# Performance work log

Measured on AMD Instinct MI355X. Metric: run time of the kernel, lower is better.

Reference implementation:

```python
import jax, jax.numpy as jnp
import numpy as np

H = 1024      # hidden_dim
P = 8         # n_paths
K = 2         # top_k
THR = 0.1     # firing_threshold
B = 16384     # batch of tokens


def setup_inputs() -> dict:
    key = jax.random.key(0)
    ks = jax.random.split(key, 8)
    g = lambda k, shape, s=0.02: (jax.random.normal(k, shape, dtype=jnp.float32) * s)
    return {
        "x": jax.random.normal(ks[0], (B, H), dtype=jnp.float32),
        # PathGate: Linear(H, H//2) -> SiLU -> Linear(H//2, P), softmax
        "gate_w1": g(ks[1], (H, H // 2)),
        "gate_b1": jnp.zeros((H // 2,), jnp.float32),
        "gate_w2": g(ks[2], (H // 2, P)),
        "gate_b2": jnp.zeros((P,), jnp.float32),
        # each path: Linear(H,H)+SiLU (stacked over P)
        "path_w": g(ks[3], (P, H, H)),
        "path_b": jnp.zeros((P, H), jnp.float32),
        # out_projs: Linear(H,H,bias=False) per path
        "proj_w": g(ks[4], (P, H, H)),
        # blend scalar parameter (init 0.0 -> alpha = 0.5)
        "blend": jnp.zeros((), jnp.float32),
    }


def reference(x, gate_w1, gate_b1, gate_w2, gate_b2, path_w, path_b, proj_w, blend):
    Bn = x.shape[0]
    # gate probabilities (B, P)
    h = jax.nn.silu(x @ gate_w1 + gate_b1)
    gate = jax.nn.softmax(h @ gate_w2 + gate_b2, axis=-1)

    # hard top-k with firing threshold -> per-token per-path combine weight
    vals, idx = jax.lax.top_k(gate, K)              # (B, K)
    fired = vals > THR                              # (B, K)
    w = jnp.zeros_like(gate).at[jnp.arange(Bn)[:, None], idx].add(
        jnp.where(fired, vals, 0.0))                # (B, P) sparse combine weights

    # path compute (dense over P; same values as masked per-path dispatch)
    path_out = jax.nn.silu(jnp.einsum('bh,phd->pbd', x, path_w) + path_b[:, None, :])
    proj_out = jnp.einsum('pbd,pdo->pbo', path_out, proj_w)   # (P, B, H)

    combined = jnp.einsum('bp,pbo->bo', w, proj_out)          # weighted scatter-combine
    total = w.sum(axis=-1)                                    # (B,)
    has_fired = total > 0
    denom = jnp.where(has_fired, total, 1.0)[:, None]
    combined = jnp.where(has_fired[:, None], combined / denom, x)

    alpha = jax.nn.sigmoid(blend)
    out = alpha * combined + (1.0 - alpha) * x
    return out, gate
```

## Files before the change

kernel.cpp:

```cpp
#include <hip/hip_runtime.h>
#include <hip/hip_bf16.h>
#include <cstdint>

#define B_TOK 16384
#define HDIM  1024
#define HGATE 512
#define NPATH 8
#define THRV  0.1f
#define RESSCALE 512.0f
#define MAXROWS (2 * B_TOK + NPATH * 128)

typedef __bf16 bf16x8 __attribute__((ext_vector_type(8)));
typedef _Float16 f16x8 __attribute__((ext_vector_type(8)));
typedef float  f32x4  __attribute__((ext_vector_type(4)));
typedef unsigned short u16;

__device__ __forceinline__ u16 f2bf(float f) {
    uint32_t u = __float_as_uint(f);
    u += 0x7fff + ((u >> 16) & 1);
    return (u16)(u >> 16);
}
__device__ __forceinline__ float bf2f(u16 v) {
    return __uint_as_float((uint32_t)v << 16);
}
union H16 { _Float16 h; u16 u; };
__device__ __forceinline__ u16 f2h(float f) { H16 t; t.h = (_Float16)f; return t.u; }
__device__ __forceinline__ float h2f(u16 b) { H16 t; t.u = b; return (float)t.h; }
__device__ __forceinline__ float silu_f(float a) {
    return a / (1.0f + expf(-a));
}
__device__ __forceinline__ f32x4 mfma_bf16(bf16x8 a, bf16x8 b, f32x4 c) {
    return __builtin_amdgcn_mfma_f32_16x16x32_bf16(a, b, c, 0, 0, 0);
}
__device__ __forceinline__ f32x4 mfma_f16(f16x8 a, f16x8 b, f32x4 c) {
    return __builtin_amdgcn_mfma_f32_16x16x32_f16(a, b, c, 0, 0, 0);
}
__device__ __forceinline__ void async_lds16(const u16* g, u16* l) {
    __builtin_amdgcn_global_load_lds((const __attribute__((address_space(1))) uint32_t*)g,
                                     (__attribute__((address_space(3))) uint32_t*)l,
                                     16, 0, 0);
}

#define PIPE_WAIT_BARRIER(N)                                             \
    do {                                                                 \
        asm volatile("s_waitcnt vmcnt(" #N ")\n\ts_barrier" ::: "memory"); \
        __builtin_amdgcn_sched_barrier(0);                               \
    } while (0)
#define PIPE_BARRIER() asm volatile("s_barrier" ::: "memory")

#define SWZ(r) (((r) >> 1) & 3)

__global__ void k_convert_x(const float* __restrict__ x, u16* __restrict__ xb,
                            u16* __restrict__ xh, u16* __restrict__ xl) {
    int i = (blockIdx.x * 256 + threadIdx.x) * 4;
    float4 v = *(const float4*)(x + i);
    float vv[4] = {v.x, v.y, v.z, v.w};
    u16 hb[4], hh[4], hl[4];
    #pragma unroll
    for (int c = 0; c < 4; c++) {
        hb[c] = f2bf(vv[c]);
        u16 hi = f2h(vv[c]);
        hh[c] = hi;
        hl[c] = f2h((vv[c] - h2f(hi)) * RESSCALE);
    }
    uint2 ob, oh, ol;
    ob.x = (uint32_t)hb[0] | ((uint32_t)hb[1] << 16);
    ob.y = (uint32_t)hb[2] | ((uint32_t)hb[3] << 16);
    oh.x = (uint32_t)hh[0] | ((uint32_t)hh[1] << 16);
    oh.y = (uint32_t)hh[2] | ((uint32_t)hh[3] << 16);
    ol.x = (uint32_t)hl[0] | ((uint32_t)hl[1] << 16);
    ol.y = (uint32_t)hl[2] | ((uint32_t)hl[3] << 16);
    *(uint2*)(xb + i) = ob;
    *(uint2*)(xh + i) = oh;
    *(uint2*)(xl + i) = ol;
}

__global__ void k_transpose_bf16(const float* __restrict__ W, u16* __restrict__ WT) {
    __shared__ float tile[32][33];
    int p = blockIdx.z;
    const float* Wp = W + (size_t)p * HDIM * HDIM;
    u16* WTp = WT + (size_t)p * HDIM * HDIM;
    int d0 = blockIdx.x * 32, h0 = blockIdx.y * 32;
    int tx = threadIdx.x, ty = threadIdx.y;
    #pragma unroll
    for (int rr = 0; rr < 4; rr++) {
        int r = ty + rr * 8;
        tile[r][tx] = Wp[(size_t)(h0 + r) * HDIM + d0 + tx];
    }
    __syncthreads();
    #pragma unroll
    for (int rr = 0; rr < 4; rr++) {
        int r = ty + rr * 8;
        WTp[(size_t)(d0 + r) * HDIM + h0 + tx] = f2bf(tile[tx][r]);
    }
}

__global__ void k_split_w1(const float* __restrict__ W1, u16* __restrict__ WhT,
                           u16* __restrict__ WlT) {
    __shared__ float tile[32][33];
    int n0 = blockIdx.x * 32, k0 = blockIdx.y * 32;
    int tx = threadIdx.x, ty = threadIdx.y;
    #pragma unroll
    for (int rr = 0; rr < 4; rr++) {
        int r = ty + rr * 8;
        tile[r][tx] = W1[(size_t)(k0 + r) * HGATE + n0 + tx];
    }
    __syncthreads();
    #pragma unroll
    for (int rr = 0; rr < 4; rr++) {
        int r = ty + rr * 8;
        float v = tile[tx][r];
        u16 hi = f2h(v);
        WhT[(size_t)(n0 + r) * HDIM + k0 + tx] = hi;
        WlT[(size_t)(n0 + r) * HDIM + k0 + tx] = f2h((v - h2f(hi)) * RESSCALE);
    }
}

__global__ __launch_bounds__(256) void k_gate_mfma(const u16* __restrict__ Ah,
                                                   const u16* __restrict__ Al,
                                                   const u16* __restrict__ BhT,
                                                   const u16* __restrict__ BlT,
                                                   const float* __restrict__ b1,
                                                   float* __restrict__ Hout) {
    __shared__ __align__(16) u16 smem[32768];
    int t = threadIdx.x;
    int m0 = blockIdx.x * 128, n0 = blockIdx.y * 128;
    int wave = t >> 6, lane = t & 63;
    int quad = lane >> 4, l16 = lane & 15;
    int wr = (wave >> 1) * 64, wc = (wave & 1) * 64;
    f32x4 acc[4][4] = {};
    f32x4 accm[4][4] = {};
    union UV { uint4 u; f16x8 v; };
    int rb = t >> 2;
    int cs = ((t & 3) ^ SWZ(rb)) * 8;
    int wb = wave * 512;

    int offA[4], offB[4];
    #pragma unroll
    for (int i = 0; i < 4; i++) {
        int rA = wr + i * 16 + l16;
        offA[i] = rA * 32 + (quad ^ SWZ(rA)) * 8;
        int rB = wc + i * 16 + l16;
        offB[i] = rB * 32 + (quad ^ SWZ(rB)) * 8;
    }

    const u16* pAh0 = Ah + (size_t)(m0 + rb) * HDIM + cs;
    const u16* pAh1 = Ah + (size_t)(m0 + 64 + rb) * HDIM + cs;
    const u16* pAl0 = Al + (size_t)(m0 + rb) * HDIM + cs;
    const u16* pAl1 = Al + (size_t)(m0 + 64 + rb) * HDIM + cs;
    const u16* pBh0 = BhT + (size_t)(n0 + rb) * HDIM + cs;
    const u16* pBh1 = BhT + (size_t)(n0 + 64 + rb) * HDIM + cs;
    const u16* pBl0 = BlT + (size_t)(n0 + rb) * HDIM + cs;
    const u16* pBl1 = BlT + (size_t)(n0 + 64 + rb) * HDIM + cs;

    auto stage = [&](int buf, int kt) {
        u16* s = smem + buf * 16384;
        int ko = kt * 32;
        async_lds16(pAh0 + ko, s + wb);
        async_lds16(pAh1 + ko, s + 2048 + wb);
        async_lds16(pAl0 + ko, s + 4096 + wb);
        async_lds16(pAl1 + ko, s + 6144 + wb);
        async_lds16(pBh0 + ko, s + 8192 + wb);
        async_lds16(pBh1 + ko, s + 10240 + wb);
        async_lds16(pBl0 + ko, s + 12288 + wb);
        async_lds16(pBl1 + ko, s + 14336 + wb);
    };
    auto compute = [&](int buf) {
        u16* s = smem + buf * 16384;
        u16* lAh = s;
        u16* lAl = s + 4096;
        u16* lBh = s + 8192;
        u16* lBl = s + 12288;
        f16x8 avh[4], avl[4], bvh[4], bvl[4];
        #pragma unroll
        for (int i = 0; i < 4; i++) {
            UV u0; u0.u = *(uint4*)(lAh + offA[i]); avh[i] = u0.v;
            UV u1; u1.u = *(uint4*)(lAl + offA[i]); avl[i] = u1.v;
            UV u2; u2.u = *(uint4*)(lBh + offB[i]); bvh[i] = u2.v;
            UV u3; u3.u = *(uint4*)(lBl + offB[i]); bvl[i] = u3.v;
        }
        #pragma unroll
        for (int i = 0; i < 4; i++)
            #pragma unroll
            for (int j = 0; j < 4; j++) {
                acc[i][j]  = mfma_f16(avh[i], bvh[j], acc[i][j]);
                accm[i][j] = mfma_f16(avh[i], bvl[j], accm[i][j]);
                accm[i][j] = mfma_f16(avl[i], bvh[j], accm[i][j]);
            }
    };

    stage(0, 0);
    for (int kt = 0; kt < 31; kt++) {
        stage((kt + 1) & 1, kt + 1);
        PIPE_WAIT_BARRIER(8);
        compute(kt & 1);
        PIPE_BARRIER();
    }
    PIPE_WAIT_BARRIER(0);
    compute(1);
    PIPE_BARRIER();

    const float inv_s = 1.0f / RESSCALE;
    float* smf = (float*)smem;
    #pragma unroll
    for (int half = 0; half < 2; half++) {
        if ((wave >> 1) == half) {
            #pragma unroll
            for (int j = 0; j < 4; j++) {
                float bj = b1[n0 + wc + j * 16 + l16];
                #pragma unroll
                for (int i = 0; i < 4; i++)
                    #pragma unroll
                    for (int r = 0; r < 4; r++) {
                        int rrow = i * 16 + quad * 4 + r;
                        float v = acc[i][j][r] + accm[i][j][r] * inv_s + bj;
                        smf[rrow * 128 + wc + j * 16 + l16] = silu_f(v);
                    }
            }
        }
        __syncthreads();
        #pragma unroll
        for (int it = 0; it < 8; it++) {
            int c = t + it * 256;
            int row = c >> 5, c4 = (c & 31) * 4;
            *(float4*)(Hout + (size_t)(m0 + half * 64 + row) * HGATE + n0 + c4) =
                *(float4*)(smf + c * 4);
        }
        __syncthreads();
    }
}

__global__ __launch_bounds__(256) void k_gate_topk(const float* __restrict__ Hin,
                                                   const float* __restrict__ W2,
                                                   const float* __restrict__ b2,
                                                   float* __restrict__ gate_out,
                                                   float* __restrict__ wnorm,
                                                   int* __restrict__ counts,
                                                   int* __restrict__ tokens,
                                                   uint32_t* __restrict__ slots) {
    __shared__ float w2t[NPATH * HGATE];
    __shared__ int cnt[NPATH];
    __shared__ int baseS[NPATH];
    __shared__ unsigned short tloc[NPATH][64];
    __shared__ uint32_t sloc[64][2];
    int t = threadIdx.x;
    #pragma unroll
    for (int j = 0; j < 16; j++) {
        int i = t + j * 256;
        w2t[(i & 7) * HGATE + (i >> 3)] = W2[i];
    }
    if (t < NPATH) cnt[t] = 0;
    __syncthreads();
    int wave = t >> 6, lane = t & 63;
    #pragma unroll 1
    for (int it = 0; it < 16; it++) {
        int tl = wave * 16 + it;
        int token = blockIdx.x * 64 + tl;
        const float* hrow = Hin + (size_t)token * HGATE;
        float hv[8];
        {
            float4 h0 = *(const float4*)(hrow + lane * 8);
            float4 h1 = *(const float4*)(hrow + lane * 8 + 4);
            hv[0] = h0.x; hv[1] = h0.y; hv[2] = h0.z; hv[3] = h0.w;
            hv[4] = h1.x; hv[5] = h1.y; hv[6] = h1.z; hv[7] = h1.w;
        }
        float logit[8];
        #pragma unroll
        for (int p = 0; p < 8; p++) {
            float s = 0.0f;
            #pragma unroll
            for (int kk = 0; kk < 8; kk++) s += hv[kk] * w2t[p * HGATE + lane * 8 + kk];
            #pragma unroll
            for (int off = 32; off >= 1; off >>= 1) s += __shfl_xor(s, off);
            logit[p] = s + b2[p];
        }
        float mx = logit[0];
        #pragma unroll
        for (int p = 1; p < 8; p++) mx = fmaxf(mx, logit[p]);
        float pr[8], sum = 0.0f;
        #pragma unroll
        for (int p = 0; p < 8; p++) { pr[p] = expf(logit[p] - mx); sum += pr[p]; }
        float inv = 1.0f / sum;
        #pragma unroll
        for (int p = 0; p < 8; p++) pr[p] *= inv;
        int i0 = 0; float v0 = pr[0];
        #pragma unroll
        for (int p = 1; p < 8; p++) { if (pr[p] > v0) { v0 = pr[p]; i0 = p; } }
        int i1 = -1; float v1 = -1.0f;
        #pragma unroll
        for (int p = 0; p < 8; p++) { if (p != i0 && pr[p] > v1) { v1 = pr[p]; i1 = p; } }
        float w0 = (v0 > THRV) ? v0 : 0.0f;
        float w1 = (v1 > THRV) ? v1 : 0.0f;
        float total = w0 + w1;
        float invden = (total > 0.0f) ? (1.0f / total) : 1.0f;
        if (lane < 8) {
            float prl = pr[0];
            #pragma unroll
            for (int p = 1; p < 8; p++) prl = (lane == p) ? pr[p] : prl;
            float wl = 0.0f;
            if (lane == i0) wl = w0 * invden;
            if (lane == i1) wl = w1 * invden;
            gate_out[(size_t)token * 8 + lane] = prl;
            wnorm[(size_t)token * 8 + lane] = wl;
        }
        if (lane == 0) {
            uint32_t e0 = 0xFFFFFFFFu, e1 = 0xFFFFFFFFu;
            if (w0 > 0.0f) {
                int j0 = atomicAdd(&cnt[i0], 1);
                tloc[i0][j0] = (unsigned short)tl;
                e0 = ((uint32_t)i0 << 16) | (uint32_t)j0;
            }
            if (w1 > 0.0f) {
                int j1 = atomicAdd(&cnt[i1], 1);
                tloc[i1][j1] = (unsigned short)tl;
                e1 = ((uint32_t)i1 << 16) | (uint32_t)j1;
            }
            sloc[tl][0] = e0; sloc[tl][1] = e1;
        }
    }
    __syncthreads();
    if (t < NPATH) baseS[t] = atomicAdd(&counts[t], cnt[t]);
    __syncthreads();
    for (int p = 0; p < NPATH; p++) {
        int n = cnt[p], b = baseS[p];
        for (int j = t; j < n; j += 256)
            tokens[p * B_TOK + b + j] = blockIdx.x * 64 + tloc[p][j];
    }
    if (t < 64) {
        #pragma unroll
        for (int s = 0; s < 2; s++) {
            uint32_t e = sloc[t][s];
            if (e != 0xFFFFFFFFu) {
                int p = e >> 16;
                int j = (int)(e & 0xFFFFu) + baseS[p];
                e = ((uint32_t)p << 16) | (uint32_t)j;
            }
            slots[(size_t)(blockIdx.x * 64 + t) * 2 + s] = e;
        }
    }
}

__global__ void k_prefix(const int* __restrict__ counts, int* __restrict__ poffs) {
    if (threadIdx.x == 0) {
        int o = 0; poffs[0] = 0;
        for (int p = 0; p < NPATH; p++) {
            o += ((counts[p] + 127) >> 7) << 7;
            poffs[p + 1] = o;
        }
    }
}

__global__ __launch_bounds__(256) void k_path1(const u16* __restrict__ A,
                                               const u16* __restrict__ WT,
                                               const float* __restrict__ pb,
                                               u16* __restrict__ hid,
                                               const int* __restrict__ counts,
                                               const int* __restrict__ tokens,
                                               const int* __restrict__ poffs) {
    int p = blockIdx.z;
    int count = counts[p];
    int m0 = blockIdx.x * 128;
    if (m0 >= count) return;
    int n0 = blockIdx.y * 128;
    int base = poffs[p];
    const u16* BT = WT + (size_t)p * HDIM * HDIM;
    const float* bias = pb + (size_t)p * HDIM;

    __shared__ __align__(16) u16 smem[24576];
    __shared__ int idx[128];
    int t = threadIdx.x;
    if (t < 128) {
        int j = m0 + t; if (j > count - 1) j = count - 1;
        idx[t] = tokens[p * B_TOK + j];
    }
    __syncthreads();
    int rb = t >> 2;
    int rowA0 = idx[rb], rowA1 = idx[64 + rb];
    int wave = t >> 6, lane = t & 63;
    int quad = lane >> 4, l16 = lane & 15;
    int wr = (wave >> 1) * 64, wc = (wave & 1) * 64;
    f32x4 acc[4][4] = {};
    union UV { uint4 u; bf16x8 v; };
    int cs = ((t & 3) ^ SWZ(rb)) * 8;
    int wb = wave * 512;

    int offA[4], offB[4];
    #pragma unroll
    for (int i = 0; i < 4; i++) {
        int rA = wr + i * 16 + l16;
        offA[i] = rA * 32 + (quad ^ SWZ(rA)) * 8;
        int rB = wc + i * 16 + l16;
        offB[i] = rB * 32 + (quad ^ SWZ(rB)) * 8;
    }

    const u16* pA0 = A + (size_t)rowA0 * HDIM + cs;
    const u16* pA1 = A + (size_t)rowA1 * HDIM + cs;
    const u16* pB0 = BT + (size_t)(n0 + rb) * HDIM + cs;
    const u16* pB1 = BT + (size_t)(n0 + 64 + rb) * HDIM + cs;

    auto stage = [&](int buf, int kt) {
        u16* s = smem + buf * 8192;
        int ko = kt * 32;
        async_lds16(pA0 + ko, s + wb);
        async_lds16(pA1 + ko, s + 2048 + wb);
        async_lds16(pB0 + ko, s + 4096 + wb);
        async_lds16(pB1 + ko, s + 6144 + wb);
    };
    auto compute = [&](int buf) {
        u16* lA = smem + buf * 8192;
        u16* lB = lA + 4096;
        bf16x8 av[4], bv[4];
        #pragma unroll
        for (int i = 0; i < 4; i++) {
            UV ua; ua.u = *(uint4*)(lA + offA[i]); av[i] = ua.v;
            UV ub; ub.u = *(uint4*)(lB + offB[i]); bv[i] = ub.v;
        }
        #pragma unroll
        for (int i = 0; i < 4; i++)
            #pragma unroll
            for (int j = 0; j < 4; j++)
                acc[i][j] = mfma_bf16(av[i], bv[j], acc[i][j]);
    };

    stage(0, 0);
    stage(1, 1);
    for (int kt = 0; kt < 30; kt++) {
        stage((kt + 2) % 3, kt + 2);
        PIPE_WAIT_BARRIER(8);
        compute(kt % 3);
        PIPE_BARRIER();
    }
    PIPE_WAIT_BARRIER(4);
    compute(0);
    PIPE_WAIT_BARRIER(0);
    compute(1);
    PIPE_BARRIER();

    #pragma unroll
    for (int j = 0; j < 4; j++) {
        float bj = bias[n0 + wc + j * 16 + l16];
        #pragma unroll
        for (int i = 0; i < 4; i++)
            #pragma unroll
            for (int r = 0; r < 4; r++) {
                int rrow = wr + i * 16 + quad * 4 + r;
                smem[rrow * 128 + wc + j * 16 + l16] = f2bf(silu_f(acc[i][j][r] + bj));
            }
    }
    __syncthreads();
    #pragma unroll
    for (int it = 0; it < 8; it++) {
        int c = t + it * 256;
        int row = c >> 4, cc = (c & 15) * 8;
        *(uint4*)(hid + (size_t)(base + m0 + row) * HDIM + n0 + cc) = *(uint4*)(smem + c * 8);
    }
}

__global__ __launch_bounds__(256) void k_path2(const u16* __restrict__ hid,
                                               const u16* __restrict__ WT,
                                               const float* __restrict__ wnorm,
                                               u16* __restrict__ pcomp,
                                               const int* __restrict__ counts,
                                               const int* __restrict__ tokens,
                                               const int* __restrict__ poffs) {
    int p = blockIdx.z;
    int count = counts[p];
    int m0 = blockIdx.x * 128;
    if (m0 >= count) return;
    int n0 = blockIdx.y * 128;
    int base = poffs[p];
    const u16* A = hid + (size_t)base * HDIM;
    const u16* BT = WT + (size_t)p * HDIM * HDIM;

    __shared__ __align__(16) u16 smem[24576];
    __shared__ float wv[128];
    int t = threadIdx.x;
    if (t < 128) {
        int j = m0 + t; if (j > count - 1) j = count - 1;
        int tok = tokens[p * B_TOK + j];
        wv[t] = wnorm[(size_t)tok * NPATH + p];
    }
    __syncthreads();
    int rb = t >> 2;
    int wave = t >> 6, lane = t & 63;
    int quad = lane >> 4, l16 = lane & 15;
    int wr = (wave >> 1) * 64, wc = (wave & 1) * 64;
    f32x4 acc[4][4] = {};
    union UV { uint4 u; bf16x8 v; };
    int cs = ((t & 3) ^ SWZ(rb)) * 8;
    int wb = wave * 512;

    int offA[4], offB[4];
    #pragma unroll
    for (int i = 0; i < 4; i++) {
        int rA = wr + i * 16 + l16;
        offA[i] = rA * 32 + (quad ^ SWZ(rA)) * 8;
        int rB = wc + i * 16 + l16;
        offB[i] = rB * 32 + (quad ^ SWZ(rB)) * 8;
    }

    const u16* pA0 = A + (size_t)(m0 + rb) * HDIM + cs;
    const u16* pA1 = A + (size_t)(m0 + 64 + rb) * HDIM + cs;
    const u16* pB0 = BT + (size_t)(n0 + rb) * HDIM + cs;
    const u16* pB1 = BT + (size_t)(n0 + 64 + rb) * HDIM + cs;

    auto stage = [&](int buf, int kt) {
        u16* s = smem + buf * 8192;
        int ko = kt * 32;
        async_lds16(pA0 + ko, s + wb);
        async_lds16(pA1 + ko, s + 2048 + wb);
        async_lds16(pB0 + ko, s + 4096 + wb);
        async_lds16(pB1 + ko, s + 6144 + wb);
    };
    auto compute = [&](int buf) {
        u16* lA = smem + buf * 8192;
        u16* lB = lA + 4096;
        bf16x8 av[4], bv[4];
        #pragma unroll
        for (int i = 0; i < 4; i++) {
            UV ua; ua.u = *(uint4*)(lA + offA[i]); av[i] = ua.v;
            UV ub; ub.u = *(uint4*)(lB + offB[i]); bv[i] = ub.v;
        }
        #pragma unroll
        for (int i = 0; i < 4; i++)
            #pragma unroll
            for (int j = 0; j < 4; j++)
                acc[i][j] = mfma_bf16(av[i], bv[j], acc[i][j]);
    };

    stage(0, 0);
    stage(1, 1);
    for (int kt = 0; kt < 30; kt++) {
        stage((kt + 2) % 3, kt + 2);
        PIPE_WAIT_BARRIER(8);
        compute(kt % 3);
        PIPE_BARRIER();
    }
    PIPE_WAIT_BARRIER(4);
    compute(0);
    PIPE_WAIT_BARRIER(0);
    compute(1);
    PIPE_BARRIER();

    #pragma unroll
    for (int j = 0; j < 4; j++) {
        #pragma unroll
        for (int i = 0; i < 4; i++)
            #pragma unroll
            for (int r = 0; r < 4; r++) {
                int rrow = wr + i * 16 + quad * 4 + r;
                smem[rrow * 128 + wc + j * 16 + l16] = f2bf(wv[rrow] * acc[i][j][r]);
            }
    }
    __syncthreads();
    #pragma unroll
    for (int it = 0; it < 8; it++) {
        int c = t + it * 256;
        int row = c >> 4, cc = (c & 15) * 8;
        *(uint4*)(pcomp + (size_t)(base + m0 + row) * HDIM + n0 + cc) = *(uint4*)(smem + c * 8);
    }
}

__global__ __launch_bounds__(256) void k_blend2(const float* __restrict__ x,
                                                const u16* __restrict__ pcomp,
                                                const uint32_t* __restrict__ slots,
                                                const int* __restrict__ poffs,
                                                const float* __restrict__ blendp,
                                                float* __restrict__ out) {
    int t = threadIdx.x, wave = t >> 6, lane = t & 63;
    int token = blockIdx.x * 4 + wave;
    float alpha = 1.0f / (1.0f + expf(-blendp[0]));
    float beta = 1.0f - alpha;
    uint32_t s0 = slots[(size_t)token * 2];
    uint32_t s1 = slots[(size_t)token * 2 + 1];
    bool f0 = (s0 != 0xFFFFFFFFu), f1 = (s1 != 0xFFFFFFFFu);
    size_t r0 = 0, r1 = 0;
    if (f0) { int p = s0 >> 16, j = s0 & 0xFFFF; r0 = (size_t)(poffs[p] + j) * HDIM; }
    if (f1) { int p = s1 >> 16, j = s1 & 0xFFFF; r1 = (size_t)(poffs[p] + j) * HDIM; }
    const float* xrow = x + (size_t)token * HDIM;
    float* orow = out + (size_t)token * HDIM;
    #pragma unroll
    for (int c = 0; c < 4; c++) {
        int col = c * 256 + lane * 4;
        float4 xv = *(const float4*)(xrow + col);
        float4 o;
        if (f0) {
            uint2 u0 = *(const uint2*)(pcomp + r0 + col);
            float a0 = bf2f(u0.x & 0xFFFF), a1 = bf2f(u0.x >> 16);
            float a2 = bf2f(u0.y & 0xFFFF), a3 = bf2f(u0.y >> 16);
            if (f1) {
                uint2 u1 = *(const uint2*)(pcomp + r1 + col);
                a0 += bf2f(u1.x & 0xFFFF); a1 += bf2f(u1.x >> 16);
                a2 += bf2f(u1.y & 0xFFFF); a3 += bf2f(u1.y >> 16);
            }
            o.x = alpha * a0 + beta * xv.x;
            o.y = alpha * a1 + beta * xv.y;
            o.z = alpha * a2 + beta * xv.z;
            o.w = alpha * a3 + beta * xv.w;
        } else {
            o = xv;
        }
        *(float4*)(orow + col) = o;
    }
}

extern "C" void kernel_launch(void* const* d_in, const int* in_sizes, int n_in,
                              void* d_out, int out_size, void* d_ws, size_t ws_size,
                              hipStream_t stream) {
    const float* x   = (const float*)d_in[0];
    const float* gw1 = (const float*)d_in[1];
    const float* gb1 = (const float*)d_in[2];
    const float* gw2 = (const float*)d_in[3];
    const float* gb2 = (const float*)d_in[4];
    const float* pw  = (const float*)d_in[5];
    const float* pb  = (const float*)d_in[6];
    const float* prw = (const float*)d_in[7];
    const float* blend = (const float*)d_in[8];
    float* out = (float*)d_out;
    float* gate_out = out + (size_t)B_TOK * HDIM;

    char* w = (char*)d_ws;
    size_t o = 0;
    u16* xb      = (u16*)(w + o);   o += (size_t)B_TOK * HDIM * 2;
    u16* pathWT  = (u16*)(w + o);   o += (size_t)NPATH * HDIM * HDIM * 2;
    u16* projWT  = (u16*)(w + o);   o += (size_t)NPATH * HDIM * HDIM * 2;
    u16* w1hT    = (u16*)(w + o);   o += (size_t)HGATE * HDIM * 2;
    u16* w1lT    = (u16*)(w + o);   o += (size_t)HGATE * HDIM * 2;
    size_t uni = o;
    float* hbuf  = (float*)(w + uni);
    u16* pcomp   = (u16*)(w + uni);
    size_t hbuf_sz  = (size_t)B_TOK * HGATE * 4;
    size_t pcomp_sz = (size_t)MAXROWS * HDIM * 2;
    o += (hbuf_sz > pcomp_sz ? hbuf_sz : pcomp_sz);
    size_t uni2 = o;
    u16* xh16    = (u16*)(w + uni2);
    u16* xl16    = (u16*)(w + uni2 + (size_t)B_TOK * HDIM * 2);
    u16* hid     = (u16*)(w + uni2);
    o += (size_t)MAXROWS * HDIM * 2;
    float* wnorm = (float*)(w + o); o += (size_t)B_TOK * NPATH * 4;
    int* tokens  = (int*)(w + o);   o += (size_t)NPATH * B_TOK * 4;
    uint32_t* slots = (uint32_t*)(w + o); o += (size_t)B_TOK * 2 * 4;
    int* counts  = (int*)(w + o);   o += 64;
    int* poffs   = (int*)(w + o);   o += 64;

    hipMemsetAsync(counts, 0, NPATH * sizeof(int), stream);
    k_convert_x<<<dim3((B_TOK * HDIM) / 1024), dim3(256), 0, stream>>>(x, xb, xh16, xl16);
    k_split_w1<<<dim3(HGATE / 32, HDIM / 32), dim3(32, 8), 0, stream>>>(gw1, w1hT, w1lT);
    k_transpose_bf16<<<dim3(32, 32, 8), dim3(32, 8), 0, stream>>>(pw, pathWT);
    k_transpose_bf16<<<dim3(32, 32, 8), dim3(32, 8), 0, stream>>>(prw, projWT);
    k_gate_mfma<<<dim3(B_TOK / 128, HGATE / 128), dim3(256), 0, stream>>>(
        xh16, xl16, w1hT, w1lT, gb1, hbuf);
    k_gate_topk<<<dim3(B_TOK / 64), dim3(256), 0, stream>>>(hbuf, gw2, gb2, gate_out,
                                                            wnorm, counts, tokens, slots);
    k_prefix<<<dim3(1), dim3(64), 0, stream>>>(counts, poffs);
    k_path1<<<dim3(128, 8, 8), dim3(256), 0, stream>>>(xb, pathWT, pb, hid,
                                                       counts, tokens, poffs);
    k_path2<<<dim3(128, 8, 8), dim3(256), 0, stream>>>(hid, projWT, wnorm, pcomp,
                                                       counts, tokens, poffs);
    k_blend2<<<dim3(B_TOK / 4), dim3(256), 0, stream>>>(x, pcomp, slots, poffs, blend, out);
}
```

Baseline: 598.7 us.

## Load GEMM operands directly from global into registers, bypassing LDS staging

Both path GEMM kernels drop the three-stage async LDS pipeline and instead have each lane load its MFMA fragments straight from global memory into registers, double-buffered across k-steps. This removes the LDS round trip, the barriers and the shared-memory footprint, which may raise occupancy. In exchange, operand data is no longer shared within the block through LDS, so each wave fetches its A and B fragments separately from global or L2. The loads are also narrow strided 16-byte reads, which risks lower memory efficiency.

```diff
diff --git a/kernel.cpp b/kernel.cpp
--- a/kernel.cpp
+++ b/kernel.cpp
@@ -366,7 +366,7 @@
     const u16* BT = WT + (size_t)p * HDIM * HDIM;
     const float* bias = pb + (size_t)p * HDIM;
 
-    __shared__ __align__(16) u16 smem[24576];
+    __shared__ __align__(16) u16 smem[16384];
     __shared__ int idx[128];
     int t = threadIdx.x;
     if (t < 128) {
@@ -374,67 +374,49 @@
         idx[t] = tokens[p * B_TOK + j];
     }
     __syncthreads();
-    int rb = t >> 2;
-    int rowA0 = idx[rb], rowA1 = idx[64 + rb];
     int wave = t >> 6, lane = t & 63;
     int quad = lane >> 4, l16 = lane & 15;
     int wr = (wave >> 1) * 64, wc = (wave & 1) * 64;
     f32x4 acc[4][4] = {};
-    union UV { uint4 u; bf16x8 v; };
-    int cs = ((t & 3) ^ SWZ(rb)) * 8;
-    int wb = wave * 512;
-
-    int offA[4], offB[4];
-    #pragma unroll
-    for (int i = 0; i < 4; i++) {
-        int rA = wr + i * 16 + l16;
-        offA[i] = rA * 32 + (quad ^ SWZ(rA)) * 8;
-        int rB = wc + i * 16 + l16;
-        offB[i] = rB * 32 + (quad ^ SWZ(rB)) * 8;
-    }
-
-    const u16* pA0 = A + (size_t)rowA0 * HDIM + cs;
-    const u16* pA1 = A + (size_t)rowA1 * HDIM + cs;
-    const u16* pB0 = BT + (size_t)(n0 + rb) * HDIM + cs;
-    const u16* pB1 = BT + (size_t)(n0 + 64 + rb) * HDIM + cs;
-
-    auto stage = [&](int buf, int kt) {
-        u16* s = smem + buf * 8192;
-        int ko = kt * 32;
-        async_lds16(pA0 + ko, s + wb);
-        async_lds16(pA1 + ko, s + 2048 + wb);
-        async_lds16(pB0 + ko, s + 4096 + wb);
-        async_lds16(pB1 + ko, s + 6144 + wb);
-    };
-    auto compute = [&](int buf) {
-        u16* lA = smem + buf * 8192;
-        u16* lB = lA + 4096;
-        bf16x8 av[4], bv[4];
-        #pragma unroll
-        for (int i = 0; i < 4; i++) {
-            UV ua; ua.u = *(uint4*)(lA + offA[i]); av[i] = ua.v;
-            UV ub; ub.u = *(uint4*)(lB + offB[i]); bv[i] = ub.v;
-        }
+
+    const u16* pa[4];
+    const u16* pbv[4];
+    #pragma unroll
+    for (int i = 0; i < 4; i++)
+        pa[i] = A + (size_t)idx[wr + i * 16 + l16] * HDIM + quad * 8;
+    #pragma unroll
+    for (int j = 0; j < 4; j++)
+        pbv[j] = BT + (size_t)(n0 + wc + j * 16 + l16) * HDIM + quad * 8;
+
+    bf16x8 a0[4], b0[4], a1[4], b1[4];
+    #pragma unroll
+    for (int i = 0; i < 4; i++) a0[i] = *(const bf16x8*)(pa[i]);
+    #pragma unroll
+    for (int j = 0; j < 4; j++) b0[j] = *(const bf16x8*)(pbv[j]);
+
+    #pragma unroll 1
+    for (int kt = 0; kt < 32; kt += 2) {
+        #pragma unroll
+        for (int i = 0; i < 4; i++) a1[i] = *(const bf16x8*)(pa[i] + (kt + 1) * 32);
+        #pragma unroll
+        for (int j = 0; j < 4; j++) b1[j] = *(const bf16x8*)(pbv[j] + (kt + 1) * 32);
         #pragma unroll
         for (int i = 0; i < 4; i++)
             #pragma unroll
             for (int j = 0; j < 4; j++)
-                acc[i][j] = mfma_bf16(av[i], bv[j], acc[i][j]);
-    };
-
-    stage(0, 0);
-    stage(1, 1);
-    for (int kt = 0; kt < 30; kt++) {
-        stage((kt + 2) % 3, kt + 2);
-        PIPE_WAIT_BARRIER(8);
-        compute(kt % 3);
-        PIPE_BARRIER();
-    }
-    PIPE_WAIT_BARRIER(4);
-    compute(0);
-    PIPE_WAIT_BARRIER(0);
-    compute(1);
-    PIPE_BARRIER();
+                acc[i][j] = mfma_bf16(a0[i], b0[j], acc[i][j]);
+        if (kt + 2 < 32) {
+            #pragma unroll
+            for (int i = 0; i < 4; i++) a0[i] = *(const bf16x8*)(pa[i] + (kt + 2) * 32);
+            #pragma unroll
+            for (int j = 0; j < 4; j++) b0[j] = *(const bf16x8*)(pbv[j] + (kt + 2) * 32);
+        }
+        #pragma unroll
+        for (int i = 0; i < 4; i++)
+            #pragma unroll
+            for (int j = 0; j < 4; j++)
+                acc[i][j] = mfma_bf16(a1[i], b1[j], acc[i][j]);
+    }
 
     #pragma unroll
     for (int j = 0; j < 4; j++) {
@@ -472,7 +454,7 @@
     const u16* A = hid + (size_t)base * HDIM;
     const u16* BT = WT + (size_t)p * HDIM * HDIM;
 
-    __shared__ __align__(16) u16 smem[24576];
+    __shared__ __align__(16) u16 smem[16384];
     __shared__ float wv[128];
     int t = threadIdx.x;
     if (t < 128) {
@@ -481,66 +463,49 @@
         wv[t] = wnorm[(size_t)tok * NPATH + p];
     }
     __syncthreads();
-    int rb = t >> 2;
     int wave = t >> 6, lane = t & 63;
     int quad = lane >> 4, l16 = lane & 15;
     int wr = (wave >> 1) * 64, wc = (wave & 1) * 64;
     f32x4 acc[4][4] = {};
-    union UV { uint4 u; bf16x8 v; };
-    int cs = ((t & 3) ^ SWZ(rb)) * 8;
-    int wb = wave * 512;
-
-    int offA[4], offB[4];
-    #pragma unroll
-    for (int i = 0; i < 4; i++) {
-        int rA = wr + i * 16 + l16;
-        offA[i] = rA * 32 + (quad ^ SWZ(rA)) * 8;
-        int rB = wc + i * 16 + l16;
-        offB[i] = rB * 32 + (quad ^ SWZ(rB)) * 8;
-    }
-
-    const u16* pA0 = A + (size_t)(m0 + rb) * HDIM + cs;
-    const u16* pA1 = A + (size_t)(m0 + 64 + rb) * HDIM + cs;
-    const u16* pB0 = BT + (size_t)(n0 + rb) * HDIM + cs;
-    const u16* pB1 = BT + (size_t)(n0 + 64 + rb) * HDIM + cs;
-
-    auto stage = [&](int buf, int kt) {
-        u16* s = smem + buf * 8192;
-        int ko = kt * 32;
-        async_lds16(pA0 + ko, s + wb);
-        async_lds16(pA1 + ko, s + 2048 + wb);
-        async_lds16(pB0 + ko, s + 4096 + wb);
-        async_lds16(pB1 + ko, s + 6144 + wb);
-    };
-    auto compute = [&](int buf) {
-        u16* lA = smem + buf * 8192;
-        u16* lB = lA + 4096;
-        bf16x8 av[4], bv[4];
-        #pragma unroll
-        for (int i = 0; i < 4; i++) {
-            UV ua; ua.u = *(uint4*)(lA + offA[i]); av[i] = ua.v;
-            UV ub; ub.u = *(uint4*)(lB + offB[i]); bv[i] = ub.v;
-        }
+
+    const u16* pa[4];
+    const u16* pbv[4];
+    #pragma unroll
+    for (int i = 0; i < 4; i++)
+        pa[i] = A + (size_t)(m0 + wr + i * 16 + l16) * HDIM + quad * 8;
+    #pragma unroll
+    for (int j = 0; j < 4; j++)
+        pbv[j] = BT + (size_t)(n0 + wc + j * 16 + l16) * HDIM + quad * 8;
+
+    bf16x8 a0[4], b0[4], a1[4], b1[4];
+    #pragma unroll
+    for (int i = 0; i < 4; i++) a0[i] = *(const bf16x8*)(pa[i]);
+    #pragma unroll
+    for (int j = 0; j < 4; j++) b0[j] = *(const bf16x8*)(pbv[j]);
+
+    #pragma unroll 1
+    for (int kt = 0; kt < 32; kt += 2) {
+        #pragma unroll
+        for (int i = 0; i < 4; i++) a1[i] = *(const bf16x8*)(pa[i] + (kt + 1) * 32);
+        #pragma unroll
+        for (int j = 0; j < 4; j++) b1[j] = *(const bf16x8*)(pbv[j] + (kt + 1) * 32);
         #pragma unroll
         for (int i = 0; i < 4; i++)
             #pragma unroll
             for (int j = 0; j < 4; j++)
-                acc[i][j] = mfma_bf16(av[i], bv[j], acc[i][j]);
-    };
-
-    stage(0, 0);
-    stage(1, 1);
-    for (int kt = 0; kt < 30; kt++) {
-        stage((kt + 2) % 3, kt + 2);
-        PIPE_WAIT_BARRIER(8);
-        compute(kt % 3);
-        PIPE_BARRIER();
-    }
-    PIPE_WAIT_BARRIER(4);
-    compute(0);
-    PIPE_WAIT_BARRIER(0);
-    compute(1);
-    PIPE_BARRIER();
+                acc[i][j] = mfma_bf16(a0[i], b0[j], acc[i][j]);
+        if (kt + 2 < 32) {
+            #pragma unroll
+            for (int i = 0; i < 4; i++) a0[i] = *(const bf16x8*)(pa[i] + (kt + 2) * 32);
+            #pragma unroll
+            for (int j = 0; j < 4; j++) b0[j] = *(const bf16x8*)(pbv[j] + (kt + 2) * 32);
+        }
+        #pragma unroll
+        for (int i = 0; i < 4; i++)
+            #pragma unroll
+            for (int j = 0; j < 4; j++)
+                acc[i][j] = mfma_bf16(a1[i], b1[j], acc[i][j]);
+    }
 
     #pragma unroll
     for (int j = 0; j < 4; j++) {
```

Result: slower. 969.9 us (+62.0%).
